# Kernel optimization log

Hardware: AMD Instinct MI355X
Metric: run time of the kernel (lower is better)

## Reference

```python
import jax, jax.numpy as jnp
import numpy as np

N = 100000      # nodes
E = 1600000     # edges (before self-loops)
F_IN = 512      # input features
H = 8           # heads layer 1
D = 8           # per-head dim layer 1
C = 40          # classes (layer 2 out, heads=1)
NEG_SLOPE = 0.2 # PyG GATConv default negative_slope


def setup_inputs() -> dict:
    key = jax.random.key(0)
    ks = jax.random.split(key, 10)
    x = jax.random.normal(ks[0], (N, F_IN), jnp.float32)
    edge_index = jax.random.randint(ks[1], (2, E), 0, N, dtype=jnp.int32)
    W1 = jax.random.normal(ks[2], (F_IN, H * D), jnp.float32) / np.float32(np.sqrt(F_IN))
    att_src1 = jax.random.normal(ks[3], (H, D), jnp.float32) / np.float32(np.sqrt(D))
    att_dst1 = jax.random.normal(ks[4], (H, D), jnp.float32) / np.float32(np.sqrt(D))
    b1 = jnp.zeros((H * D,), jnp.float32)
    W2 = jax.random.normal(ks[5], (H * D, C), jnp.float32) / np.float32(np.sqrt(H * D))
    att_src2 = jax.random.normal(ks[6], (1, C), jnp.float32) / np.float32(np.sqrt(C))
    att_dst2 = jax.random.normal(ks[7], (1, C), jnp.float32) / np.float32(np.sqrt(C))
    b2 = jnp.zeros((C,), jnp.float32)
    return {"x": x, "edge_index": edge_index, "W1": W1, "att_src1": att_src1,
            "att_dst1": att_dst1, "b1": b1, "W2": W2, "att_src2": att_src2,
            "att_dst2": att_dst2, "b2": b2}


def _gat_layer(x, src, dst, W, a_src, a_dst, heads, dim):
    # Dense projection, then per-head attention logits.
    h = (x @ W).reshape(-1, heads, dim)            # [N, H, D]
    alpha_s = jnp.einsum('nhd,hd->nh', h, a_src)   # [N, H]
    alpha_d = jnp.einsum('nhd,hd->nh', h, a_dst)
    e = jax.nn.leaky_relu(alpha_s[src] + alpha_d[dst], NEG_SLOPE)  # [E, H]
    # Segment softmax over edges grouped by destination node.
    emax = jax.ops.segment_max(e, dst, num_segments=N)
    emax = jnp.where(jnp.isfinite(emax), emax, 0.0)
    ee = jnp.exp(e - emax[dst])
    denom = jax.ops.segment_sum(ee, dst, num_segments=N)
    alpha = ee / (denom[dst] + 1e-16)              # [E, H]
    # Scatter-aggregate weighted neighbor features.
    msg = h[src] * alpha[:, :, None]               # [E, H, D]
    return jax.ops.segment_sum(msg, dst, num_segments=N)  # [N, H, D]


def reference(x, edge_index, W1, att_src1, att_dst1, b1, W2, att_src2, att_dst2, b2):
    # PyG GATConv adds self-loops by default.
    loops = jnp.arange(N, dtype=edge_index.dtype)
    src = jnp.concatenate([edge_index[0], loops])
    dst = jnp.concatenate([edge_index[1], loops])
    # Layer 1: 8 heads, concat=True, then ELU. (dropouts identity in eval mode)
    h1 = _gat_layer(x, src, dst, W1, att_src1, att_dst1, H, D).reshape(N, H * D) + b1
    h1 = jax.nn.elu(h1)
    # Layer 2: 1 head, concat=False -> mean over heads (trivial for H=1).
    h2 = _gat_layer(h1, src, dst, W2, att_src2, att_dst2, 1, C)[:, 0, :] + b2
    return jax.nn.log_softmax(h2, axis=1)
```

## Files before the change

kernel.cpp:

```cpp
#include <hip/hip_runtime.h>

#define F_IN   512
#define HD     64
#define NHEAD  8
#define NC     40
#define NEG    0.2f

typedef __attribute__((ext_vector_type(8))) short bf16x8;
typedef __attribute__((ext_vector_type(4))) float f32x4;

__device__ __forceinline__ float lrelu(float x) { return x > 0.0f ? x : NEG * x; }

__device__ __forceinline__ short f2bf(float f) {
    unsigned u = __float_as_uint(f);
    u += 0x7FFF + ((u >> 16) & 1);
    return (short)(u >> 16);
}
__device__ __forceinline__ float bf2f(short h) {
    return __uint_as_float(((unsigned)(unsigned short)h) << 16);
}

__global__ void count_kernel(const int* __restrict__ dst, int* __restrict__ deg,
                             int* __restrict__ pos, int E) {
    int e = blockIdx.x * 256 + threadIdx.x;
    if (e < E) pos[e] = atomicAdd(&deg[dst[e]], 1);
}

__global__ __launch_bounds__(256) void scanA_kernel(const int* __restrict__ deg,
                                                    int* __restrict__ incl,
                                                    int* __restrict__ bsum, int Nn) {
    __shared__ int wsum[4];
    int t = threadIdx.x, b = blockIdx.x;
    int base = b * 1024 + t * 4;
    int v0 = (base + 0) < Nn ? deg[base + 0] : 0;
    int v1 = (base + 1) < Nn ? deg[base + 1] : 0;
    int v2 = (base + 2) < Nn ? deg[base + 2] : 0;
    int v3 = (base + 3) < Nn ? deg[base + 3] : 0;
    int p0 = v0, p1 = p0 + v1, p2 = p1 + v2, p3 = p2 + v3;
    int lane = t & 63, w = t >> 6;
    int sc = p3;
    for (int off = 1; off < 64; off <<= 1) {
        int u = __shfl_up(sc, off);
        if (lane >= off) sc += u;
    }
    if (lane == 63) wsum[w] = sc;
    __syncthreads();
    int woff = 0;
#pragma unroll
    for (int i = 0; i < 4; ++i) if (i < w) woff += wsum[i];
    int excl = woff + sc - p3;
    if (base + 0 < Nn) incl[base + 0] = excl + p0;
    if (base + 1 < Nn) incl[base + 1] = excl + p1;
    if (base + 2 < Nn) incl[base + 2] = excl + p2;
    if (base + 3 < Nn) incl[base + 3] = excl + p3;
    if (t == 0) bsum[b] = wsum[0] + wsum[1] + wsum[2] + wsum[3];
}

__global__ void scanB_kernel(int* __restrict__ bsum, int nb) {
    int lane = threadIdx.x;
    int a = lane < nb ? bsum[lane] : 0;
    int c = (lane + 64) < nb ? bsum[lane + 64] : 0;
    int sa = a, sc2 = c;
    for (int off = 1; off < 64; off <<= 1) {
        int u = __shfl_up(sa, off);  if (lane >= off) sa += u;
        int u2 = __shfl_up(sc2, off); if (lane >= off) sc2 += u2;
    }
    int totA = __shfl(sa, 63);
    int ea = sa - a;
    int ec = totA + sc2 - c;
    if (lane < nb) bsum[lane] = ea;
    if (lane + 64 < nb) bsum[lane + 64] = ec;
}

__global__ void scanC_kernel(const int* __restrict__ incl, const int* __restrict__ bsum,
                             int* __restrict__ rp, int Nn) {
    int i = blockIdx.x * 256 + threadIdx.x;
    if (i == 0) rp[0] = 0;
    if (i < Nn) rp[i + 1] = incl[i] + bsum[i >> 10];
}

__global__ void scatter_kernel(const int* __restrict__ src, const int* __restrict__ dst,
                               const int* __restrict__ pos, const int* __restrict__ rp,
                               int* __restrict__ col, int E) {
    int e = blockIdx.x * 256 + threadIdx.x;
    if (e < E) {
        int d = dst[e];
        int p = rp[d] + pos[e];
        __builtin_nontemporal_store(src[e], &col[p]);
    }
}

#define G1_BM 128
__global__ __launch_bounds__(256) void gemm1_kernel(const float* __restrict__ X,
                                                    const float* __restrict__ W,
                                                    const float* __restrict__ att_s,
                                                    const float* __restrict__ att_d,
                                                    float* __restrict__ Hout,
                                                    float* __restrict__ as1,
                                                    float* __restrict__ ad1, int Nn) {
    __shared__ short Bh[4][HD][8];
    __shared__ short Bl[4][HD][8];
    int tid = threadIdx.x;
    int wid = tid >> 6, lane = tid & 63;
    int lrow = lane & 15, kgrp = lane >> 4;
    int row0 = blockIdx.x * G1_BM;
    int rowA = row0 + wid * 32 + lrow;

    int sc = tid & 63, skc = tid >> 6;

    float ats[4], atd[4];
#pragma unroll
    for (int fc = 0; fc < 4; ++fc) { ats[fc] = att_s[fc * 16 + lrow]; atd[fc] = att_d[fc * 16 + lrow]; }

    f32x4 acc[2][4];
#pragma unroll
    for (int fr = 0; fr < 2; ++fr)
#pragma unroll
        for (int fc = 0; fc < 4; ++fc) acc[fr][fc] = (f32x4){0.f, 0.f, 0.f, 0.f};

    float4 a_cur[2][2], a_nxt[2][2];
#pragma unroll
    for (int fr = 0; fr < 2; ++fr) {
        int gr = rowA + fr * 16;
        if (gr < Nn) {
            const float* p = X + (size_t)gr * F_IN + kgrp * 8;
            a_cur[fr][0] = *reinterpret_cast<const float4*>(p);
            a_cur[fr][1] = *reinterpret_cast<const float4*>(p + 4);
        } else {
            a_cur[fr][0] = a_cur[fr][1] = make_float4(0.f, 0.f, 0.f, 0.f);
        }
    }

    for (int it = 0; it < F_IN / 32; ++it) {
        int k0 = it * 32;
        float wreg[8];
#pragma unroll
        for (int j = 0; j < 8; ++j)
            wreg[j] = W[(size_t)(k0 + skc * 8 + j) * HD + sc];
        if (it + 1 < F_IN / 32) {
#pragma unroll
            for (int fr = 0; fr < 2; ++fr) {
                int gr = rowA + fr * 16;
                if (gr < Nn) {
                    const float* p = X + (size_t)gr * F_IN + (k0 + 32) + kgrp * 8;
                    a_nxt[fr][0] = *reinterpret_cast<const float4*>(p);
                    a_nxt[fr][1] = *reinterpret_cast<const float4*>(p + 4);
                } else {
                    a_nxt[fr][0] = a_nxt[fr][1] = make_float4(0.f, 0.f, 0.f, 0.f);
                }
            }
        }
        bf16x8 af[2];
#pragma unroll
        for (int fr = 0; fr < 2; ++fr) {
            float fs[8] = {a_cur[fr][0].x, a_cur[fr][0].y, a_cur[fr][0].z, a_cur[fr][0].w,
                           a_cur[fr][1].x, a_cur[fr][1].y, a_cur[fr][1].z, a_cur[fr][1].w};
#pragma unroll
            for (int j = 0; j < 8; ++j) af[fr][j] = f2bf(fs[j]);
        }
        __syncthreads();
        {
            bf16x8 vh, vl;
#pragma unroll
            for (int j = 0; j < 8; ++j) {
                short hh = f2bf(wreg[j]);
                vh[j] = hh;
                vl[j] = f2bf(wreg[j] - bf2f(hh));
            }
            *reinterpret_cast<bf16x8*>(&Bh[skc][sc][0]) = vh;
            *reinterpret_cast<bf16x8*>(&Bl[skc][sc][0]) = vl;
        }
        __syncthreads();
        bf16x8 bh[4], bl[4];
#pragma unroll
        for (int fc = 0; fc < 4; ++fc) {
            bh[fc] = *reinterpret_cast<const bf16x8*>(&Bh[kgrp][fc * 16 + lrow][0]);
            bl[fc] = *reinterpret_cast<const bf16x8*>(&Bl[kgrp][fc * 16 + lrow][0]);
        }
#pragma unroll
        for (int fr = 0; fr < 2; ++fr)
#pragma unroll
            for (int fc = 0; fc < 4; ++fc) {
                acc[fr][fc] = __builtin_amdgcn_mfma_f32_16x16x32_bf16(af[fr], bh[fc], acc[fr][fc], 0, 0, 0);
                acc[fr][fc] = __builtin_amdgcn_mfma_f32_16x16x32_bf16(af[fr], bl[fc], acc[fr][fc], 0, 0, 0);
            }
        if (it + 1 < F_IN / 32) {
#pragma unroll
            for (int fr = 0; fr < 2; ++fr) {
                a_cur[fr][0] = a_nxt[fr][0];
                a_cur[fr][1] = a_nxt[fr][1];
            }
        }
    }

#pragma unroll
    for (int fr = 0; fr < 2; ++fr) {
#pragma unroll
        for (int r = 0; r < 4; ++r) {
            int gr = row0 + wid * 32 + fr * 16 + kgrp * 4 + r;
            float hv[4], sp[4], dp[4];
#pragma unroll
            for (int fc = 0; fc < 4; ++fc) {
                hv[fc] = acc[fr][fc][r];
                sp[fc] = hv[fc] * ats[fc];
                dp[fc] = hv[fc] * atd[fc];
            }
#pragma unroll
            for (int mask = 1; mask <= 4; mask <<= 1) {
#pragma unroll
                for (int fc = 0; fc < 4; ++fc) {
                    sp[fc] += __shfl_xor(sp[fc], mask);
                    dp[fc] += __shfl_xor(dp[fc], mask);
                }
            }
            if (gr < Nn) {
#pragma unroll
                for (int fc = 0; fc < 4; ++fc)
                    Hout[(size_t)gr * HD + fc * 16 + lrow] = hv[fc];
                if ((lane & 7) == 0) {
                    int hh = lrow >> 3;
#pragma unroll
                    for (int fc = 0; fc < 4; ++fc) {
                        as1[gr * NHEAD + fc * 2 + hh] = sp[fc];
                        ad1[gr * NHEAD + fc * 2 + hh] = dp[fc];
                    }
                }
            }
        }
    }
}

__global__ __launch_bounds__(256) void agg1_kernel(const float* __restrict__ Hp,
                                                   const float* __restrict__ as1,
                                                   const float* __restrict__ ad1,
                                                   const int* __restrict__ col,
                                                   const int* __restrict__ rp,
                                                   const float* __restrict__ b1,
                                                   float* __restrict__ H1out, int Nn) {
    int n = blockIdx.x * 4 + (threadIdx.x >> 6);
    int lane = threadIdx.x & 63;
    if (n >= Nn) return;
    int slot = lane >> 4, l16 = lane & 15, h = l16 >> 1;
    int beg = rp[n], end = rp[n + 1];
    float adv = ad1[n * NHEAD + h];
    float4 acc = make_float4(0.f, 0.f, 0.f, 0.f);
    float dw = 0.f;
    for (int t = beg + slot; t < end; t += 4) {
        int s = col[t];
        float w = __expf(lrelu(as1[s * NHEAD + h] + adv));
        dw += w;
        float4 v = *reinterpret_cast<const float4*>(&Hp[(size_t)s * HD + l16 * 4]);
        acc.x += w * v.x; acc.y += w * v.y; acc.z += w * v.z; acc.w += w * v.w;
    }
#pragma unroll
    for (int mask = 16; mask < 64; mask <<= 1) {
        acc.x += __shfl_xor(acc.x, mask);
        acc.y += __shfl_xor(acc.y, mask);
        acc.z += __shfl_xor(acc.z, mask);
        acc.w += __shfl_xor(acc.w, mask);
        dw    += __shfl_xor(dw, mask);
    }
    if (slot == 0) {
        float w = __expf(lrelu(as1[n * NHEAD + h] + adv));
        float4 v = *reinterpret_cast<const float4*>(&Hp[(size_t)n * HD + l16 * 4]);
        acc.x += w * v.x; acc.y += w * v.y; acc.z += w * v.z; acc.w += w * v.w;
        dw += w;
        float invd = 1.0f / (dw + 1e-16f);
        float4 bb = *reinterpret_cast<const float4*>(&b1[l16 * 4]);
        acc.x = acc.x * invd + bb.x; acc.y = acc.y * invd + bb.y;
        acc.z = acc.z * invd + bb.z; acc.w = acc.w * invd + bb.w;
        acc.x = acc.x > 0.0f ? acc.x : __expf(acc.x) - 1.0f;
        acc.y = acc.y > 0.0f ? acc.y : __expf(acc.y) - 1.0f;
        acc.z = acc.z > 0.0f ? acc.z : __expf(acc.z) - 1.0f;
        acc.w = acc.w > 0.0f ? acc.w : __expf(acc.w) - 1.0f;
        *reinterpret_cast<float4*>(&H1out[(size_t)n * HD + l16 * 4]) = acc;
    }
}

#define G2R 64
__global__ __launch_bounds__(256) void gemm2_kernel(const float* __restrict__ H1,
                                                    const float* __restrict__ W2,
                                                    const float* __restrict__ asw,
                                                    const float* __restrict__ adw,
                                                    float* __restrict__ H2p,
                                                    float* __restrict__ as2,
                                                    float* __restrict__ ad2, int Nn) {
    __shared__ float Hs[G2R][HD + 1];
    __shared__ float W2s[HD][NC];
    __shared__ float asv[NC], adv[NC];
    int tid = threadIdx.x;
    for (int i = tid; i < HD * NC; i += 256) W2s[i / NC][i % NC] = W2[i];
    if (tid < NC) { asv[tid] = asw[tid]; adv[tid] = adw[tid]; }
    int row0 = blockIdx.x * G2R;
#pragma unroll
    for (int i = 0; i < 4; ++i) {
        int linear = i * 1024 + tid * 4;
        int r = linear >> 6, c = linear & 63;
        int gr = row0 + r;
        float4 v = make_float4(0.f, 0.f, 0.f, 0.f);
        if (gr < Nn) v = *reinterpret_cast<const float4*>(&H1[(size_t)gr * HD + c]);
        Hs[r][c + 0] = v.x; Hs[r][c + 1] = v.y; Hs[r][c + 2] = v.z; Hs[r][c + 3] = v.w;
    }
    __syncthreads();
    int row = tid >> 2, cg = tid & 3;
    int gr = row0 + row;
    float acc[10];
#pragma unroll
    for (int j = 0; j < 10; ++j) acc[j] = 0.0f;
    for (int k = 0; k < HD; ++k) {
        float a = Hs[row][k];
#pragma unroll
        for (int j = 0; j < 10; ++j) acc[j] += a * W2s[k][cg * 10 + j];
    }
    float sa = 0.0f, da = 0.0f;
#pragma unroll
    for (int j = 0; j < 10; ++j) {
        sa += acc[j] * asv[cg * 10 + j];
        da += acc[j] * adv[cg * 10 + j];
    }
    sa += __shfl_xor(sa, 1); sa += __shfl_xor(sa, 2);
    da += __shfl_xor(da, 1); da += __shfl_xor(da, 2);
    if (gr < Nn) {
        if (cg == 0) { as2[gr] = sa; ad2[gr] = da; }
        float* o = &H2p[(size_t)gr * NC + cg * 10];
#pragma unroll
        for (int j = 0; j < 10; j += 2) {
            *reinterpret_cast<float2*>(&o[j]) = make_float2(acc[j], acc[j + 1]);
        }
    }
}

__global__ __launch_bounds__(256) void agg2_kernel(const float* __restrict__ H2p,
                                                   const float* __restrict__ as2,
                                                   const float* __restrict__ ad2,
                                                   const int* __restrict__ col,
                                                   const int* __restrict__ rp,
                                                   const float* __restrict__ b2,
                                                   float* __restrict__ out, int Nn) {
    int n = blockIdx.x * 4 + (threadIdx.x >> 6);
    int lane = threadIdx.x & 63;
    if (n >= Nn) return;
    int slot = lane >> 4, l16 = lane & 15;
    bool act = l16 < 10;
    int beg = rp[n], end = rp[n + 1];
    float adv = ad2[n];
    float4 acc = make_float4(0.f, 0.f, 0.f, 0.f);
    float dw = 0.f;
    for (int t = beg + slot; t < end; t += 4) {
        int s = col[t];
        float w = __expf(lrelu(as2[s] + adv));
        dw += w;
        if (act) {
            float4 v = *reinterpret_cast<const float4*>(&H2p[(size_t)s * NC + l16 * 4]);
            acc.x += w * v.x; acc.y += w * v.y; acc.z += w * v.z; acc.w += w * v.w;
        }
    }
#pragma unroll
    for (int mask = 16; mask < 64; mask <<= 1) {
        acc.x += __shfl_xor(acc.x, mask);
        acc.y += __shfl_xor(acc.y, mask);
        acc.z += __shfl_xor(acc.z, mask);
        acc.w += __shfl_xor(acc.w, mask);
        dw    += __shfl_xor(dw, mask);
    }
    float w = __expf(lrelu(as2[n] + adv));
    dw += w;
    float invd = 1.0f / (dw + 1e-16f);
    if (act) {
        float4 v = *reinterpret_cast<const float4*>(&H2p[(size_t)n * NC + l16 * 4]);
        float4 bb = *reinterpret_cast<const float4*>(&b2[l16 * 4]);
        acc.x = (acc.x + w * v.x) * invd + bb.x;
        acc.y = (acc.y + w * v.y) * invd + bb.y;
        acc.z = (acc.z + w * v.z) * invd + bb.z;
        acc.w = (acc.w + w * v.w) * invd + bb.w;
    }
    float mloc = act ? fmaxf(fmaxf(acc.x, acc.y), fmaxf(acc.z, acc.w)) : -INFINITY;
#pragma unroll
    for (int mask = 1; mask < 16; mask <<= 1) mloc = fmaxf(mloc, __shfl_xor(mloc, mask));
    float s4 = act ? (__expf(acc.x - mloc) + __expf(acc.y - mloc) +
                      __expf(acc.z - mloc) + __expf(acc.w - mloc)) : 0.0f;
#pragma unroll
    for (int mask = 1; mask < 16; mask <<= 1) s4 += __shfl_xor(s4, mask);
    float lse = mloc + __logf(s4);
    if (slot == 0 && act) {
        float4 o = make_float4(acc.x - lse, acc.y - lse, acc.z - lse, acc.w - lse);
        *reinterpret_cast<float4*>(&out[(size_t)n * NC + l16 * 4]) = o;
    }
}

extern "C" void kernel_launch(void* const* d_in, const int* in_sizes, int n_in,
                              void* d_out, int out_size, void* d_ws, size_t ws_size,
                              hipStream_t stream) {
    const float* x    = (const float*)d_in[0];
    const int*   ei   = (const int*)d_in[1];
    const float* W1   = (const float*)d_in[2];
    const float* as1w = (const float*)d_in[3];
    const float* ad1w = (const float*)d_in[4];
    const float* b1   = (const float*)d_in[5];
    const float* W2   = (const float*)d_in[6];
    const float* as2w = (const float*)d_in[7];
    const float* ad2w = (const float*)d_in[8];
    const float* b2   = (const float*)d_in[9];
    float* out = (float*)d_out;

    int Nn = in_sizes[0] / F_IN;
    int E  = in_sizes[1] / 2;
    const int* srcv = ei;
    const int* dstv = ei + E;

    char* ws = (char*)d_ws;
    size_t off = 0;
    auto alloc = [&](size_t bytes) { size_t cur = off; off += (bytes + 255) & ~255ULL; return cur; };
    float* h1p  = (float*)(ws + alloc((size_t)Nn * HD * 4));
    float* h1   = (float*)(ws + alloc((size_t)Nn * HD * 4));
    float* as1v = (float*)(ws + alloc((size_t)Nn * NHEAD * 4));
    float* ad1v = (float*)(ws + alloc((size_t)Nn * NHEAD * 4));
    float* h2p  = (float*)(ws + alloc((size_t)Nn * NC * 4));
    float* as2v = (float*)(ws + alloc((size_t)Nn * 4));
    float* ad2v = (float*)(ws + alloc((size_t)Nn * 4));
    int* deg  = (int*)(ws + alloc((size_t)Nn * 4));
    int* incl = (int*)(ws + alloc((size_t)Nn * 4));
    int* rp   = (int*)(ws + alloc((size_t)(Nn + 1) * 4));
    int* pos  = (int*)(ws + alloc((size_t)E * 4));
    int* col  = (int*)(ws + alloc((size_t)E * 4));
    int* bsum = (int*)(ws + alloc(256 * 4));

    int nb = (Nn + 1023) / 1024;

    hipMemsetAsync(deg, 0, (size_t)Nn * 4, stream);
    count_kernel<<<(E + 255) / 256, 256, 0, stream>>>(dstv, deg, pos, E);
    scanA_kernel<<<nb, 256, 0, stream>>>(deg, incl, bsum, Nn);
    scanB_kernel<<<1, 64, 0, stream>>>(bsum, nb);
    scanC_kernel<<<(Nn + 255) / 256, 256, 0, stream>>>(incl, bsum, rp, Nn);
    scatter_kernel<<<(E + 255) / 256, 256, 0, stream>>>(srcv, dstv, pos, rp, col, E);

    gemm1_kernel<<<(Nn + G1_BM - 1) / G1_BM, 256, 0, stream>>>(x, W1, as1w, ad1w, h1p, as1v, ad1v, Nn);
    agg1_kernel<<<(Nn + 3) / 4, 256, 0, stream>>>(h1p, as1v, ad1v, col, rp, b1, h1, Nn);
    gemm2_kernel<<<(Nn + G2R - 1) / G2R, 256, 0, stream>>>(h1, W2, as2w, ad2w, h2p, as2v, ad2v, Nn);
    agg2_kernel<<<(Nn + 3) / 4, 256, 0, stream>>>(h2p, as2v, ad2v, col, rp, b2, out, Nn);
}
```

Measured before the change: 383.5 us.

## Fuse gemm2 into agg1, merge scatter into gemm1, store features as bf16

The CSR scatter is folded into the gemm1 launch as extra blocks. The layer-2 projection and its attention dots move into the agg1 epilogue, with W2 held in shared memory and the inputs broadcast by shuffles. The projected features of both layers are now stored in bf16, which halves the bytes read by the gather-heavy aggregation kernels. The memset becomes a zero kernel. This cuts kernel launches and the intermediate h1 round-trip, at the cost of reduced precision and W2 being reloaded per block.

```diff
diff --git a/kernel.cpp b/kernel.cpp
--- a/kernel.cpp
+++ b/kernel.cpp
@@ -18,6 +18,13 @@
 }
 __device__ __forceinline__ float bf2f(short h) {
     return __uint_as_float(((unsigned)(unsigned short)h) << 16);
+}
+__device__ __forceinline__ float bfl(unsigned u) { return __uint_as_float(u << 16); }
+__device__ __forceinline__ float bfh(unsigned u) { return __uint_as_float(u & 0xFFFF0000u); }
+
+__global__ void zero_kernel(int* __restrict__ p, int n) {
+    int i = blockIdx.x * 256 + threadIdx.x;
+    if (i < n) p[i] = 0;
 }
 
 __global__ void count_kernel(const int* __restrict__ dst, int* __restrict__ deg,
@@ -79,28 +86,34 @@
     if (i < Nn) rp[i + 1] = incl[i] + bsum[i >> 10];
 }
 
-__global__ void scatter_kernel(const int* __restrict__ src, const int* __restrict__ dst,
-                               const int* __restrict__ pos, const int* __restrict__ rp,
-                               int* __restrict__ col, int E) {
-    int e = blockIdx.x * 256 + threadIdx.x;
-    if (e < E) {
-        int d = dst[e];
-        int p = rp[d] + pos[e];
-        __builtin_nontemporal_store(src[e], &col[p]);
-    }
-}
-
 #define G1_BM 128
-__global__ __launch_bounds__(256) void gemm1_kernel(const float* __restrict__ X,
-                                                    const float* __restrict__ W,
-                                                    const float* __restrict__ att_s,
-                                                    const float* __restrict__ att_d,
-                                                    float* __restrict__ Hout,
-                                                    float* __restrict__ as1,
-                                                    float* __restrict__ ad1, int Nn) {
+__global__ __launch_bounds__(256) void g1s_kernel(const float* __restrict__ X,
+                                                  const float* __restrict__ W,
+                                                  const float* __restrict__ att_s,
+                                                  const float* __restrict__ att_d,
+                                                  unsigned short* __restrict__ Hp,
+                                                  float* __restrict__ as1,
+                                                  float* __restrict__ ad1,
+                                                  const int* __restrict__ src,
+                                                  const int* __restrict__ dst,
+                                                  const int* __restrict__ pos,
+                                                  const int* __restrict__ rp,
+                                                  int* __restrict__ col,
+                                                  int Nn, int E, int nG1) {
     __shared__ short Bh[4][HD][8];
     __shared__ short Bl[4][HD][8];
     int tid = threadIdx.x;
+
+    if ((int)blockIdx.x >= nG1) {
+        int e = ((int)blockIdx.x - nG1) * 256 + tid;
+        if (e < E) {
+            int d = dst[e];
+            int p = rp[d] + pos[e];
+            __builtin_nontemporal_store(src[e], &col[p]);
+        }
+        return;
+    }
+
     int wid = tid >> 6, lane = tid & 63;
     int lrow = lane & 15, kgrp = lane >> 4;
     int row0 = blockIdx.x * G1_BM;
@@ -216,7 +229,7 @@
             if (gr < Nn) {
 #pragma unroll
                 for (int fc = 0; fc < 4; ++fc)
-                    Hout[(size_t)gr * HD + fc * 16 + lrow] = hv[fc];
+                    Hp[(size_t)gr * HD + fc * 16 + lrow] = (unsigned short)f2bf(hv[fc]);
                 if ((lane & 7) == 0) {
                     int hh = lrow >> 3;
 #pragma unroll
@@ -230,27 +243,39 @@
     }
 }
 
-__global__ __launch_bounds__(256) void agg1_kernel(const float* __restrict__ Hp,
+__global__ __launch_bounds__(256) void agg1_kernel(const unsigned short* __restrict__ Hp,
                                                    const float* __restrict__ as1,
                                                    const float* __restrict__ ad1,
                                                    const int* __restrict__ col,
                                                    const int* __restrict__ rp,
                                                    const float* __restrict__ b1,
-                                                   float* __restrict__ H1out, int Nn) {
-    int n = blockIdx.x * 4 + (threadIdx.x >> 6);
-    int lane = threadIdx.x & 63;
+                                                   const float* __restrict__ W2,
+                                                   const float* __restrict__ as2w,
+                                                   const float* __restrict__ ad2w,
+                                                   unsigned int* __restrict__ h2p,
+                                                   float* __restrict__ as2,
+                                                   float* __restrict__ ad2, int Nn) {
+    __shared__ float W2s[HD][NC];
+    __shared__ float asv[NC], adv[NC];
+    int tid = threadIdx.x;
+    for (int i = tid; i < HD * NC; i += 256) W2s[i / NC][i % NC] = W2[i];
+    if (tid < NC) { asv[tid] = as2w[tid]; adv[tid] = ad2w[tid]; }
+    __syncthreads();
+    int n = blockIdx.x * 4 + (tid >> 6);
+    int lane = tid & 63;
     if (n >= Nn) return;
     int slot = lane >> 4, l16 = lane & 15, h = l16 >> 1;
     int beg = rp[n], end = rp[n + 1];
-    float adv = ad1[n * NHEAD + h];
+    float adv1 = ad1[n * NHEAD + h];
     float4 acc = make_float4(0.f, 0.f, 0.f, 0.f);
     float dw = 0.f;
     for (int t = beg + slot; t < end; t += 4) {
         int s = col[t];
-        float w = __expf(lrelu(as1[s * NHEAD + h] + adv));
+        float w = __expf(lrelu(as1[s * NHEAD + h] + adv1));
         dw += w;
-        float4 v = *reinterpret_cast<const float4*>(&Hp[(size_t)s * HD + l16 * 4]);
-        acc.x += w * v.x; acc.y += w * v.y; acc.z += w * v.z; acc.w += w * v.w;
+        uint2 u = *reinterpret_cast<const uint2*>(&Hp[(size_t)s * HD + l16 * 4]);
+        acc.x += w * bfl(u.x); acc.y += w * bfh(u.x);
+        acc.z += w * bfl(u.y); acc.w += w * bfh(u.y);
     }
 #pragma unroll
     for (int mask = 16; mask < 64; mask <<= 1) {
@@ -260,10 +285,11 @@
         acc.w += __shfl_xor(acc.w, mask);
         dw    += __shfl_xor(dw, mask);
     }
-    if (slot == 0) {
-        float w = __expf(lrelu(as1[n * NHEAD + h] + adv));
-        float4 v = *reinterpret_cast<const float4*>(&Hp[(size_t)n * HD + l16 * 4]);
-        acc.x += w * v.x; acc.y += w * v.y; acc.z += w * v.z; acc.w += w * v.w;
+    {
+        float w = __expf(lrelu(as1[n * NHEAD + h] + adv1));
+        uint2 u = *reinterpret_cast<const uint2*>(&Hp[(size_t)n * HD + l16 * 4]);
+        acc.x += w * bfl(u.x); acc.y += w * bfh(u.x);
+        acc.z += w * bfl(u.y); acc.w += w * bfh(u.y);
         dw += w;
         float invd = 1.0f / (dw + 1e-16f);
         float4 bb = *reinterpret_cast<const float4*>(&b1[l16 * 4]);
@@ -273,64 +299,30 @@
         acc.y = acc.y > 0.0f ? acc.y : __expf(acc.y) - 1.0f;
         acc.z = acc.z > 0.0f ? acc.z : __expf(acc.z) - 1.0f;
         acc.w = acc.w > 0.0f ? acc.w : __expf(acc.w) - 1.0f;
-        *reinterpret_cast<float4*>(&H1out[(size_t)n * HD + l16 * 4]) = acc;
-    }
-}
-
-#define G2R 64
-__global__ __launch_bounds__(256) void gemm2_kernel(const float* __restrict__ H1,
-                                                    const float* __restrict__ W2,
-                                                    const float* __restrict__ asw,
-                                                    const float* __restrict__ adw,
-                                                    float* __restrict__ H2p,
-                                                    float* __restrict__ as2,
-                                                    float* __restrict__ ad2, int Nn) {
-    __shared__ float Hs[G2R][HD + 1];
-    __shared__ float W2s[HD][NC];
-    __shared__ float asv[NC], adv[NC];
-    int tid = threadIdx.x;
-    for (int i = tid; i < HD * NC; i += 256) W2s[i / NC][i % NC] = W2[i];
-    if (tid < NC) { asv[tid] = asw[tid]; adv[tid] = adw[tid]; }
-    int row0 = blockIdx.x * G2R;
-#pragma unroll
-    for (int i = 0; i < 4; ++i) {
-        int linear = i * 1024 + tid * 4;
-        int r = linear >> 6, c = linear & 63;
-        int gr = row0 + r;
-        float4 v = make_float4(0.f, 0.f, 0.f, 0.f);
-        if (gr < Nn) v = *reinterpret_cast<const float4*>(&H1[(size_t)gr * HD + c]);
-        Hs[r][c + 0] = v.x; Hs[r][c + 1] = v.y; Hs[r][c + 2] = v.z; Hs[r][c + 3] = v.w;
-    }
-    __syncthreads();
-    int row = tid >> 2, cg = tid & 3;
-    int gr = row0 + row;
-    float acc[10];
-#pragma unroll
-    for (int j = 0; j < 10; ++j) acc[j] = 0.0f;
+    }
+    int cw = lane < NC ? lane : 0;
+    float h2 = 0.f;
+#pragma unroll
     for (int k = 0; k < HD; ++k) {
-        float a = Hs[row][k];
-#pragma unroll
-        for (int j = 0; j < 10; ++j) acc[j] += a * W2s[k][cg * 10 + j];
-    }
-    float sa = 0.0f, da = 0.0f;
-#pragma unroll
-    for (int j = 0; j < 10; ++j) {
-        sa += acc[j] * asv[cg * 10 + j];
-        da += acc[j] * adv[cg * 10 + j];
-    }
-    sa += __shfl_xor(sa, 1); sa += __shfl_xor(sa, 2);
-    da += __shfl_xor(da, 1); da += __shfl_xor(da, 2);
-    if (gr < Nn) {
-        if (cg == 0) { as2[gr] = sa; ad2[gr] = da; }
-        float* o = &H2p[(size_t)gr * NC + cg * 10];
-#pragma unroll
-        for (int j = 0; j < 10; j += 2) {
-            *reinterpret_cast<float2*>(&o[j]) = make_float2(acc[j], acc[j + 1]);
-        }
-    }
-}
-
-__global__ __launch_bounds__(256) void agg2_kernel(const float* __restrict__ H2p,
+        int srcl = k >> 2;
+        float comp = (k & 3) == 0 ? acc.x : (k & 3) == 1 ? acc.y : (k & 3) == 2 ? acc.z : acc.w;
+        float hk = __shfl(comp, srcl);
+        h2 += hk * W2s[k][cw];
+    }
+    float sa = lane < NC ? h2 * asv[lane] : 0.f;
+    float da = lane < NC ? h2 * adv[lane] : 0.f;
+#pragma unroll
+    for (int mask = 1; mask < 64; mask <<= 1) { sa += __shfl_xor(sa, mask); da += __shfl_xor(da, mask); }
+    if (lane == 0) { as2[n] = sa; ad2[n] = da; }
+    float hp2 = __shfl(h2, lane + 1);
+    if (lane < NC && !(lane & 1)) {
+        unsigned int u = ((unsigned int)(unsigned short)f2bf(hp2) << 16) |
+                         (unsigned short)f2bf(h2);
+        h2p[(size_t)n * 20 + (lane >> 1)] = u;
+    }
+}
+
+__global__ __launch_bounds__(256) void agg2_kernel(const unsigned int* __restrict__ h2p,
                                                    const float* __restrict__ as2,
                                                    const float* __restrict__ ad2,
                                                    const int* __restrict__ col,
@@ -351,8 +343,9 @@
         float w = __expf(lrelu(as2[s] + adv));
         dw += w;
         if (act) {
-            float4 v = *reinterpret_cast<const float4*>(&H2p[(size_t)s * NC + l16 * 4]);
-            acc.x += w * v.x; acc.y += w * v.y; acc.z += w * v.z; acc.w += w * v.w;
+            uint2 u = *reinterpret_cast<const uint2*>(&h2p[(size_t)s * 20 + l16 * 2]);
+            acc.x += w * bfl(u.x); acc.y += w * bfh(u.x);
+            acc.z += w * bfl(u.y); acc.w += w * bfh(u.y);
         }
     }
 #pragma unroll
@@ -367,12 +360,12 @@
     dw += w;
     float invd = 1.0f / (dw + 1e-16f);
     if (act) {
-        float4 v = *reinterpret_cast<const float4*>(&H2p[(size_t)n * NC + l16 * 4]);
+        uint2 u = *reinterpret_cast<const uint2*>(&h2p[(size_t)n * 20 + l16 * 2]);
         float4 bb = *reinterpret_cast<const float4*>(&b2[l16 * 4]);
-        acc.x = (acc.x + w * v.x) * invd + bb.x;
-        acc.y = (acc.y + w * v.y) * invd + bb.y;
-        acc.z = (acc.z + w * v.z) * invd + bb.z;
-        acc.w = (acc.w + w * v.w) * invd + bb.w;
+        acc.x = (acc.x + w * bfl(u.x)) * invd + bb.x;
+        acc.y = (acc.y + w * bfh(u.x)) * invd + bb.y;
+        acc.z = (acc.z + w * bfl(u.y)) * invd + bb.z;
+        acc.w = (acc.w + w * bfh(u.y)) * invd + bb.w;
     }
     float mloc = act ? fmaxf(fmaxf(acc.x, acc.y), fmaxf(acc.z, acc.w)) : -INFINITY;
 #pragma unroll
@@ -411,11 +404,10 @@
     char* ws = (char*)d_ws;
     size_t off = 0;
     auto alloc = [&](size_t bytes) { size_t cur = off; off += (bytes + 255) & ~255ULL; return cur; };
-    float* h1p  = (float*)(ws + alloc((size_t)Nn * HD * 4));
-    float* h1   = (float*)(ws + alloc((size_t)Nn * HD * 4));
+    unsigned short* Hp = (unsigned short*)(ws + alloc((size_t)Nn * HD * 2));
     float* as1v = (float*)(ws + alloc((size_t)Nn * NHEAD * 4));
     float* ad1v = (float*)(ws + alloc((size_t)Nn * NHEAD * 4));
-    float* h2p  = (float*)(ws + alloc((size_t)Nn * NC * 4));
+    unsigned int* h2p = (unsigned int*)(ws + alloc((size_t)Nn * 20 * 4));
     float* as2v = (float*)(ws + alloc((size_t)Nn * 4));
     float* ad2v = (float*)(ws + alloc((size_t)Nn * 4));
     int* deg  = (int*)(ws + alloc((size_t)Nn * 4));
@@ -425,17 +417,19 @@
     int* col  = (int*)(ws + alloc((size_t)E * 4));
     int* bsum = (int*)(ws + alloc(256 * 4));
 
-    int nb = (Nn + 1023) / 1024;
-
-    hipMemsetAsync(deg, 0, (size_t)Nn * 4, stream);
+    int nb  = (Nn + 1023) / 1024;
+    int nG1 = (Nn + G1_BM - 1) / G1_BM;
+    int nSC = (E + 255) / 256;
+
+    zero_kernel<<<(Nn + 255) / 256, 256, 0, stream>>>(deg, Nn);
     count_kernel<<<(E + 255) / 256, 256, 0, stream>>>(dstv, deg, pos, E);
     scanA_kernel<<<nb, 256, 0, stream>>>(deg, incl, bsum, Nn);
     scanB_kernel<<<1, 64, 0, stream>>>(bsum, nb);
     scanC_kernel<<<(Nn + 255) / 256, 256, 0, stream>>>(incl, bsum, rp, Nn);
-    scatter_kernel<<<(E + 255) / 256, 256, 0, stream>>>(srcv, dstv, pos, rp, col, E);
-
-    gemm1_kernel<<<(Nn + G1_BM - 1) / G1_BM, 256, 0, stream>>>(x, W1, as1w, ad1w, h1p, as1v, ad1v, Nn);
-    agg1_kernel<<<(Nn + 3) / 4, 256, 0, stream>>>(h1p, as1v, ad1v, col, rp, b1, h1, Nn);
-    gemm2_kernel<<<(Nn + G2R - 1) / G2R, 256, 0, stream>>>(h1, W2, as2w, ad2w, h2p, as2v, ad2v, Nn);
+
+    g1s_kernel<<<nG1 + nSC, 256, 0, stream>>>(x, W1, as1w, ad1w, Hp, as1v, ad1v,
+                                              srcv, dstv, pos, rp, col, Nn, E, nG1);
+    agg1_kernel<<<(Nn + 3) / 4, 256, 0, stream>>>(Hp, as1v, ad1v, col, rp, b1,
+                                                  W2, as2w, ad2w, h2p, as2v, ad2v, Nn);
     agg2_kernel<<<(Nn + 3) / 4, 256, 0, stream>>>(h2p, as2v, ad2v, col, rp, b2, out, Nn);
 }
```

Result: slower. 393.4 us (+2.6%).
